# Kernel optimization log

Hardware: AMD Instinct MI355X
Metric: run time of the kernel (lower is better)

The kernel has to match this reference:

```python
import jax, jax.numpy as jnp
import numpy as np

N_HEADS = 16


def setup_inputs() -> dict:
    key = jax.random.key(0)
    k1, k2, k3 = jax.random.split(key, 3)
    B, T, C = 4, 2048, 1024
    x = jax.random.normal(k1, (B, T, C), dtype=jnp.float32)
    # torch nn.Linear weights are (out_features, in_features); y = x @ W.T
    w_in = jax.random.normal(k2, (3 * C, C), dtype=jnp.float32) * 0.02
    w_out = jax.random.normal(k3, (C, C), dtype=jnp.float32) * 0.02
    return {"x": x, "w_in": w_in, "w_out": w_out}


def reference(x, w_in, w_out):
    B, T, C = x.shape
    H = N_HEADS
    hd = C // H

    qkv = x @ w_in.T                      # [B, T, 3C]
    q, k, v = jnp.split(qkv, 3, axis=2)   # each [B, T, C]

    def heads(t):
        return t.reshape(B, T, H, hd).transpose(0, 2, 1, 3)  # [B, H, T, hd]

    q, k, v = heads(q), heads(k), heads(v)

    scale = 1.0 / jnp.sqrt(jnp.float32(hd))
    scores = jnp.einsum('bhqd,bhkd->bhqk', q, k) * scale      # [B, H, T, T]
    causal = jnp.tril(jnp.ones((T, T), dtype=bool))
    scores = jnp.where(causal, scores, -jnp.inf)
    attn = jax.nn.softmax(scores, axis=-1)
    y = jnp.einsum('bhqk,bhkd->bhqd', attn, v)                # [B, H, T, hd]
    y = y.transpose(0, 2, 1, 3).reshape(B, T, C)
    return y @ w_out.T
```

## Files before the change

kernel.cpp:

```cpp
#include <hip/hip_runtime.h>
#include <stdint.h>

#define BB 4
#define TT 2048
#define CC 1024
#define HH 16
#define HD 64
#define C3 3072
#define MM (BB*TT)

typedef __bf16 bf16_t;
typedef bf16_t bf16x8 __attribute__((ext_vector_type(8)));
typedef float f32x4 __attribute__((ext_vector_type(4)));
typedef unsigned short u16;
typedef u16 u16x8 __attribute__((ext_vector_type(8)));
typedef uint32_t u32;

static __device__ __forceinline__ u16 f2bf(float f){
  u32 u = __builtin_bit_cast(u32, f);
  u32 r = (u + 0x7fffu + ((u >> 16) & 1u)) >> 16;
  return (u16)r;
}

static __device__ __forceinline__ f32x4 mfma16(bf16x8 a, bf16x8 b, f32x4 c){
  return __builtin_amdgcn_mfma_f32_16x16x32_bf16(a, b, c, 0, 0, 0);
}

typedef __attribute__((address_space(1))) void* gas_t;
typedef __attribute__((address_space(3))) void* las_t;
static __device__ __forceinline__ void gload16(const void* g, void* l){
  __builtin_amdgcn_global_load_lds((gas_t)g, (las_t)l, 16, 0, 0);
}

__global__ __launch_bounds__(256) void cvt_all(const float* __restrict__ x,
                                               const float* __restrict__ wi,
                                               const float* __restrict__ wo,
                                               u16* __restrict__ out){
  const int n1 = MM*CC/8, n2 = C3*CC/8, n3 = CC*CC/8;
  const int total = n1 + n2 + n3;
  int stride = gridDim.x * blockDim.x;
  for (int i = blockIdx.x * blockDim.x + threadIdx.x; i < total; i += stride){
    const float* src; int k;
    if (i < n1){ src = x; k = i; }
    else if (i < n1 + n2){ src = wi; k = i - n1; }
    else { src = wo; k = i - n1 - n2; }
    const float4* p = (const float4*)src + (size_t)k * 2;
    float4 a = p[0], b = p[1];
    u16x8 o;
    o[0]=f2bf(a.x); o[1]=f2bf(a.y); o[2]=f2bf(a.z); o[3]=f2bf(a.w);
    o[4]=f2bf(b.x); o[5]=f2bf(b.y); o[6]=f2bf(b.z); o[7]=f2bf(b.w);
    *((u16x8*)out + i) = o;
  }
}

template<int OUTBF>
__global__ __launch_bounds__(256) void gemm_bt(const u16* __restrict__ A,
                                               const u16* __restrict__ Bm,
                                               void* __restrict__ Cp,
                                               int M, int N, int K,
                                               int nbx, int cpx){
  __shared__ u16 As[128*64];
  __shared__ u16 Bs[128*64];
  const int bid = blockIdx.x;
  const int nb = (bid & 7) * cpx + (bid >> 3);
  const int by = nb / nbx, bx = nb - by * nbx;
  const int tid  = threadIdx.x;
  const int lane = tid & 63;
  const int w    = tid >> 6;
  const int m0   = by * 128;
  const int n0   = bx * 128;
  const int wm   = (w >> 1) * 64;
  const int wn   = (w & 1) * 64;
  const int lr   = lane & 15;
  const int lg4  = lane >> 4;

  f32x4 acc[4][4] = {};

  const int rq  = tid >> 3;
  const int c8s = ((tid & 7) ^ (rq & 7)) * 8;
  const u16* gA = A  + (size_t)(m0 + rq) * K + c8s;
  const u16* gB = Bm + (size_t)(n0 + rq) * K + c8s;
  char* lA = (char*)As + tid*16;
  char* lB = (char*)Bs + tid*16;

  for (int k0 = 0; k0 < K; k0 += 64){
    #pragma unroll
    for (int q = 0; q < 4; q++){
      gload16(gA + (size_t)(q*32)*K + k0, lA + q*4096);
      gload16(gB + (size_t)(q*32)*K + k0, lB + q*4096);
    }
    __syncthreads();
    #pragma unroll
    for (int kk = 0; kk < 2; kk++){
      bf16x8 af[4], bfr[4];
      #pragma unroll
      for (int m = 0; m < 4; m++){
        int row = wm + m*16 + lr;
        int slot = ((kk<<2) | lg4) ^ (row & 7);
        af[m] = *(const bf16x8*)((const char*)As + row*128 + slot*16);
      }
      #pragma unroll
      for (int n = 0; n < 4; n++){
        int row = wn + n*16 + lr;
        int slot = ((kk<<2) | lg4) ^ (row & 7);
        bfr[n] = *(const bf16x8*)((const char*)Bs + row*128 + slot*16);
      }
      #pragma unroll
      for (int m = 0; m < 4; m++)
        #pragma unroll
        for (int n = 0; n < 4; n++)
          acc[m][n] = mfma16(af[m], bfr[n], acc[m][n]);
    }
    __syncthreads();
  }

  const int cr = lg4 * 4;
  #pragma unroll
  for (int m = 0; m < 4; m++)
    #pragma unroll
    for (int n = 0; n < 4; n++)
      #pragma unroll
      for (int j = 0; j < 4; j++){
        size_t row = (size_t)(m0 + wm + m*16 + cr + j);
        size_t col = (size_t)(n0 + wn + n*16 + lr);
        if (OUTBF) ((u16*)Cp)[row*(size_t)N + col] = f2bf(acc[m][n][j]);
        else       ((float*)Cp)[row*(size_t)N + col] = acc[m][n][j];
      }
}

__global__ __launch_bounds__(256, 2) void attn_fwd(const u16* __restrict__ qkv,
                                                   u16* __restrict__ y){
  __shared__ u16 Kl[2][64*72];
  __shared__ u16 Vt[2][64*72];
  const int bid = blockIdx.x;
  const int tq = bid >> 6;
  const int h = bid & 15, b = (bid >> 4) & 3;
  const int tid = threadIdx.x, lane = tid & 63, w = tid >> 6;
  const int lr = lane & 15, lg = lane >> 4;
  const size_t base = (size_t)b * TT * C3;
  const int qA = tq*64 + w*16;
  const int qB = (31-tq)*64 + w*16;
  const float SC = 0.18033688011112042f;

  bf16x8 qf[2][2];
  {
    const u16* qp0 = qkv + base + (size_t)(qA + lr) * C3 + h*HD;
    qf[0][0] = *(const bf16x8*)(qp0 + lg*8);
    qf[0][1] = *(const bf16x8*)(qp0 + 32 + lg*8);
    const u16* qp1 = qkv + base + (size_t)(qB + lr) * C3 + h*HD;
    qf[1][0] = *(const bf16x8*)(qp1 + lg*8);
    qf[1][1] = *(const bf16x8*)(qp1 + 32 + lg*8);
    #pragma unroll
    for (int m = 0; m < 2; m++)
      #pragma unroll
      for (int i = 0; i < 2; i++)
        #pragma unroll
        for (int e = 0; e < 8; e++)
          qf[m][i][e] = (bf16_t)((float)qf[m][i][e] * SC);
  }

  const int rK = tid >> 3, cK = tid & 7;
  const int rp = tid & 15;
  const int dc = (tid >> 4) & 7;
  const int hf = tid >> 7;
  const u16* gK = qkv + base + (size_t)rK * C3 + CC + h*HD + cK*8;
  const u16* gV = qkv + base + (size_t)(2*rp + 32*hf) * C3 + 2*CC + h*HD + dc*8;

  const int kkey = ((rK >> 3) & 1) << 5;
  const int kw0 = rK*72 + ((cK*8) ^ kkey);
  const int kw1 = (rK+32)*72 + ((cK*8) ^ kkey);
  const int vcol = (2*rp + 32*hf) ^ (8*dc);

  const int rdx = ((lr >> 2) & 1) << 5;
  const int rbase = 8*(lr >> 2) + (lr & 3);

  u16x8 kreg[2], vreg[2];
  kreg[0] = *(const u16x8*)(gK);
  kreg[1] = *(const u16x8*)(gK + (size_t)32*C3);
  vreg[0] = *(const u16x8*)(gV);
  vreg[1] = *(const u16x8*)(gV + C3);

  f32x4 o[2][4] = {};
  float mj[2] = {-1e30f, -1e30f};
  float lj[2] = {0.f, 0.f};

  const int ktmax = 31 - tq;
  for (int kt = 0; kt <= ktmax; kt++){
    const int cb = kt & 1;
    u16* KL = Kl[cb];
    u16* VT = Vt[cb];
    *(u16x8*)&KL[kw0] = kreg[0];
    *(u16x8*)&KL[kw1] = kreg[1];
    #pragma unroll
    for (int e = 0; e < 8; e++){
      u32 pk = (u32)vreg[0][e] | ((u32)vreg[1][e] << 16);
      *(u32*)&VT[(dc*8+e)*72 + vcol] = pk;
    }
    __syncthreads();

    if (kt < ktmax){
      const u16* gk2 = gK + (size_t)(kt+1)*64*C3;
      const u16* gv2 = gV + (size_t)(kt+1)*64*C3;
      kreg[0] = *(const u16x8*)(gk2);
      kreg[1] = *(const u16x8*)(gk2 + (size_t)32*C3);
      vreg[0] = *(const u16x8*)(gv2);
      vreg[1] = *(const u16x8*)(gv2 + C3);
    }

    const bool m0act = (kt <= tq);
    bf16x8 vb[8];

    #pragma unroll
    for (int m = 1; m >= 0; m--){
      if (m == 0 && !m0act) continue;

      f32x4 s[4] = {};
      __builtin_amdgcn_s_setprio(1);
      #pragma unroll
      for (int n = 0; n < 4; n++){
        const int rho = 32*(n>>1) + 4*(n&1) + rbase;
        bf16x8 kb0 = *(const bf16x8*)&KL[rho*72 + ((     lg*8) ^ rdx)];
        bf16x8 kb1 = *(const bf16x8*)&KL[rho*72 + ((32 + lg*8) ^ rdx)];
        s[n] = mfma16(kb0, qf[m][0], s[n]);
        s[n] = mfma16(kb1, qf[m][1], s[n]);
      }
      __builtin_amdgcn_s_setprio(0);

      if (m == 1){
        #pragma unroll
        for (int n = 0; n < 4; n++){
          const int dcr = (2*n + (lr >> 3)) & 7;
          const int c0 = (lg ^ dcr) * 8;
          vb[2*n]   = *(const bf16x8*)&VT[(n*16+lr)*72 + c0];
          vb[2*n+1] = *(const bf16x8*)&VT[(n*16+lr)*72 + (c0 ^ 32)];
        }
      }

      const int qrow = (m ? qB : qA) + lr;
      const bool dm = (kt == (m ? ktmax : tq));
      if (dm){
        #pragma unroll
        for (int n = 0; n < 4; n++)
          #pragma unroll
          for (int j = 0; j < 4; j++)
            if (kt*64 + 32*(n>>1) + 8*lg + 4*(n&1) + j > qrow)
              s[n][j] = -1e30f;
      }
      float x0 = fmaxf(fmaxf(s[0][0], s[0][1]), fmaxf(s[0][2], s[0][3]));
      float x1 = fmaxf(fmaxf(s[1][0], s[1][1]), fmaxf(s[1][2], s[1][3]));
      float x2 = fmaxf(fmaxf(s[2][0], s[2][1]), fmaxf(s[2][2], s[2][3]));
      float x3 = fmaxf(fmaxf(s[3][0], s[3][1]), fmaxf(s[3][2], s[3][3]));
      float tm = fmaxf(fmaxf(x0, x1), fmaxf(x2, x3));
      tm = fmaxf(tm, __shfl_xor(tm, 16, 64));
      tm = fmaxf(tm, __shfl_xor(tm, 32, 64));
      float mo = mj[m];
      if (!__all(tm <= mo + 4.0f)){
        float mn = fmaxf(mo, tm);
        float al = __builtin_amdgcn_exp2f(mo - mn);
        mj[m] = mn;
        lj[m] *= al;
        float a0 = __shfl(al, lg*4+0, 16);
        float a1 = __shfl(al, lg*4+1, 16);
        float a2 = __shfl(al, lg*4+2, 16);
        float a3 = __shfl(al, lg*4+3, 16);
        #pragma unroll
        for (int n = 0; n < 4; n++){
          o[m][n][0] *= a0; o[m][n][1] *= a1;
          o[m][n][2] *= a2; o[m][n][3] *= a3;
        }
      }
      float mm = mj[m];
      float psn[4];
      bf16x8 pa, pb;
      #pragma unroll
      for (int n = 0; n < 4; n++){
        float p0 = __builtin_amdgcn_exp2f(s[n][0] - mm);
        float p1 = __builtin_amdgcn_exp2f(s[n][1] - mm);
        float p2 = __builtin_amdgcn_exp2f(s[n][2] - mm);
        float p3 = __builtin_amdgcn_exp2f(s[n][3] - mm);
        psn[n] = (p0 + p1) + (p2 + p3);
        if (n == 0){ pa[0]=(bf16_t)p0; pa[1]=(bf16_t)p1; pa[2]=(bf16_t)p2; pa[3]=(bf16_t)p3; }
        if (n == 1){ pa[4]=(bf16_t)p0; pa[5]=(bf16_t)p1; pa[6]=(bf16_t)p2; pa[7]=(bf16_t)p3; }
        if (n == 2){ pb[0]=(bf16_t)p0; pb[1]=(bf16_t)p1; pb[2]=(bf16_t)p2; pb[3]=(bf16_t)p3; }
        if (n == 3){ pb[4]=(bf16_t)p0; pb[5]=(bf16_t)p1; pb[6]=(bf16_t)p2; pb[7]=(bf16_t)p3; }
      }
      float ps = (psn[0] + psn[1]) + (psn[2] + psn[3]);
      ps += __shfl_xor(ps, 16, 64);
      ps += __shfl_xor(ps, 32, 64);
      lj[m] += ps;

      __builtin_amdgcn_s_setprio(1);
      #pragma unroll
      for (int n = 0; n < 4; n++){
        o[m][n] = mfma16(pa, vb[2*n],   o[m][n]);
        o[m][n] = mfma16(pb, vb[2*n+1], o[m][n]);
      }
      __builtin_amdgcn_s_setprio(0);
    }
  }

  #pragma unroll
  for (int m = 0; m < 2; m++){
    float inv = 1.0f / lj[m];
    float i0 = __shfl(inv, lg*4+0, 16);
    float i1 = __shfl(inv, lg*4+1, 16);
    float i2 = __shfl(inv, lg*4+2, 16);
    float i3 = __shfl(inv, lg*4+3, 16);
    const int qb = (m ? qB : qA);
    #pragma unroll
    for (int j = 0; j < 4; j++){
      float ij = (j==0) ? i0 : (j==1) ? i1 : (j==2) ? i2 : i3;
      size_t row = (size_t)b*TT + qb + lg*4 + j;
      #pragma unroll
      for (int n = 0; n < 4; n++)
        y[row*CC + h*HD + n*16 + lr] = f2bf(o[m][n][j] * ij);
    }
  }
}

extern "C" void kernel_launch(void* const* d_in, const int* in_sizes, int n_in,
                              void* d_out, int out_size, void* d_ws, size_t ws_size,
                              hipStream_t stream){
  const float* x     = (const float*)d_in[0];
  const float* w_in  = (const float*)d_in[1];
  const float* w_out = (const float*)d_in[2];
  float* out = (float*)d_out;

  u16* xb   = (u16*)d_ws;
  u16* wib  = xb  + (size_t)MM * CC;
  u16* wob  = wib + (size_t)C3 * CC;
  u16* qkvb = wob + (size_t)CC * CC;
  u16* yb   = xb;

  cvt_all<<<2048, 256, 0, stream>>>(x, w_in, w_out, xb);

  gemm_bt<1><<<1536, 256, 0, stream>>>(xb, wib, (void*)qkvb, MM, C3, CC, 24, 192);
  attn_fwd<<<1024, 256, 0, stream>>>(qkvb, yb);
  gemm_bt<0><<<512, 256, 0, stream>>>(yb, wob, (void*)out, MM, CC, CC, 8, 64);
}
```

Before: 165.1 us.

## Use 256x256 double-buffered tile GEMM with 512 threads for QKV projection

Adds a new GEMM kernel for the QKV projection that uses 256x256 output tiles, 8 waves per block, and double-buffered shared memory. Global loads for the next K-tile are interleaved with MFMA phases, and the kernel uses barriers and priority hints. The larger tiles raise arithmetic intensity and cut redundant global reads relative to the 128x128 kernel. The costs are a larger LDS footprint (128KB per block), heavy register use for the 8x4 accumulators, and only 384 blocks, which may underfill 256 CUs at 2 blocks per CU.

Measured after the change: 175.7 us. +6.4%, slower.

```diff
diff --git a/kernel.cpp b/kernel.cpp
--- a/kernel.cpp
+++ b/kernel.cpp
@@ -51,6 +51,110 @@
     o[4]=f2bf(b.x); o[5]=f2bf(b.y); o[6]=f2bf(b.z); o[7]=f2bf(b.w);
     *((u16x8*)out + i) = o;
   }
+}
+
+__global__ __launch_bounds__(512, 2) void gemm_bt256(const u16* __restrict__ A,
+                                                     const u16* __restrict__ Bm,
+                                                     u16* __restrict__ Cp,
+                                                     int N, int K,
+                                                     int nbx, int cpx){
+  __shared__ u16 As[2][256*64];
+  __shared__ u16 Bs[2][256*64];
+  const int bid = blockIdx.x;
+  const int nb = (bid & 7) * cpx + (bid >> 3);
+  const int by = nb / nbx, bx = nb - by * nbx;
+  const int tid = threadIdx.x;
+  const int lane = tid & 63;
+  const int w = tid >> 6;
+  const int m0g = by * 256, n0g = bx * 256;
+  const int wm = (w >> 2) * 128;
+  const int wn = (w & 3) * 64;
+  const int lr = lane & 15;
+  const int lg4 = lane >> 4;
+
+  f32x4 acc[8][4] = {};
+
+  const int rq  = tid >> 3;
+  const int c8s = ((tid & 7) ^ (rq & 7)) * 8;
+  const u16* gA = A  + (size_t)(m0g + rq) * K + c8s;
+  const u16* gB = Bm + (size_t)(n0g + rq) * K + c8s;
+
+  auto stage2 = [&](int buf, int t1, int q){
+    gload16(gA + (size_t)(q*64)*K + t1*64, (char*)&As[buf][0] + q*8192 + tid*16);
+    gload16(gB + (size_t)(q*64)*K + t1*64, (char*)&Bs[buf][0] + q*8192 + tid*16);
+  };
+  auto lda = [&](int buf, int m, int kk)->bf16x8{
+    int row = wm + m*16 + lr;
+    int slot = ((kk<<2) | lg4) ^ (row & 7);
+    return *(const bf16x8*)((const char*)&As[buf][0] + row*128 + slot*16);
+  };
+  auto ldb = [&](int buf, int n, int kk)->bf16x8{
+    int row = wn + n*16 + lr;
+    int slot = ((kk<<2) | lg4) ^ (row & 7);
+    return *(const bf16x8*)((const char*)&Bs[buf][0] + row*128 + slot*16);
+  };
+
+  #pragma unroll
+  for (int q = 0; q < 4; q++) stage2(0, 0, q);
+
+  const int NT = K >> 6;
+  for (int t = 0; t < NT; t++){
+    const int c = t & 1;
+    const bool pf = (t + 1 < NT);
+    bf16x8 bfr[4][2];
+
+    if (pf){ stage2(c^1, t+1, 0); asm volatile("s_waitcnt vmcnt(2)" ::: "memory"); }
+    else   {                      asm volatile("s_waitcnt vmcnt(0)" ::: "memory"); }
+    __builtin_amdgcn_s_barrier();
+    __builtin_amdgcn_sched_barrier(0);
+    #pragma unroll
+    for (int n = 0; n < 4; n++){ bfr[n][0] = ldb(c,n,0); bfr[n][1] = ldb(c,n,1); }
+    {
+      bf16x8 a00 = lda(c,0,0), a01 = lda(c,0,1);
+      bf16x8 a10 = lda(c,1,0), a11 = lda(c,1,1);
+      __builtin_amdgcn_s_setprio(1);
+      #pragma unroll
+      for (int n = 0; n < 4; n++){
+        acc[0][n] = mfma16(a00, bfr[n][0], acc[0][n]);
+        acc[0][n] = mfma16(a01, bfr[n][1], acc[0][n]);
+        acc[1][n] = mfma16(a10, bfr[n][0], acc[1][n]);
+        acc[1][n] = mfma16(a11, bfr[n][1], acc[1][n]);
+      }
+      __builtin_amdgcn_s_setprio(0);
+    }
+    __builtin_amdgcn_s_barrier();
+
+    #pragma unroll
+    for (int p = 1; p < 4; p++){
+      bf16x8 a00 = lda(c,2*p,0),   a01 = lda(c,2*p,1);
+      bf16x8 a10 = lda(c,2*p+1,0), a11 = lda(c,2*p+1,1);
+      if (pf) stage2(c^1, t+1, p);
+      __builtin_amdgcn_s_barrier();
+      __builtin_amdgcn_sched_barrier(0);
+      __builtin_amdgcn_s_setprio(1);
+      #pragma unroll
+      for (int n = 0; n < 4; n++){
+        acc[2*p][n]   = mfma16(a00, bfr[n][0], acc[2*p][n]);
+        acc[2*p][n]   = mfma16(a01, bfr[n][1], acc[2*p][n]);
+        acc[2*p+1][n] = mfma16(a10, bfr[n][0], acc[2*p+1][n]);
+        acc[2*p+1][n] = mfma16(a11, bfr[n][1], acc[2*p+1][n]);
+      }
+      __builtin_amdgcn_s_setprio(0);
+      __builtin_amdgcn_s_barrier();
+    }
+  }
+
+  const int cr = lg4 * 4;
+  #pragma unroll
+  for (int m = 0; m < 8; m++)
+    #pragma unroll
+    for (int n = 0; n < 4; n++)
+      #pragma unroll
+      for (int j = 0; j < 4; j++){
+        size_t row = (size_t)(m0g + wm + m*16 + cr + j);
+        size_t col = (size_t)(n0g + wn + n*16 + lr);
+        Cp[row*(size_t)N + col] = f2bf(acc[m][n][j]);
+      }
 }
 
 template<int OUTBF>
@@ -334,7 +438,7 @@
 
   cvt_all<<<2048, 256, 0, stream>>>(x, w_in, w_out, xb);
 
-  gemm_bt<1><<<1536, 256, 0, stream>>>(xb, wib, (void*)qkvb, MM, C3, CC, 24, 192);
+  gemm_bt256<<<384, 512, 0, stream>>>(xb, wib, qkvb, C3, CC, 12, 48);
   attn_fwd<<<1024, 256, 0, stream>>>(qkvb, yb);
   gemm_bt<0><<<512, 256, 0, stream>>>(yb, wob, (void*)out, MM, CC, CC, 8, 64);
 }
```

## Stage two K/V tiles per barrier in attention loop

Applied to the files above, without the earlier changes.

The attention kernel now moves two 64-key tiles of K and V into shared memory per loop iteration, double-buffered, instead of one. The goal is to halve the number of block-wide barriers and to issue larger, deeper global prefetches that overlap more with compute. In exchange, shared memory per block doubles to about 74 KB and prefetch register use doubles. That may lower occupancy or cause register spills under the two-blocks-per-CU launch bound. When the number of key tiles is odd, the last iteration also loads one extra tile it never uses.

Result: slower. 168.4 us (+2.0%).

```diff
diff --git a/kernel.cpp b/kernel.cpp
--- a/kernel.cpp
+++ b/kernel.cpp
@@ -130,8 +130,8 @@
 
 __global__ __launch_bounds__(256, 2) void attn_fwd(const u16* __restrict__ qkv,
                                                    u16* __restrict__ y){
-  __shared__ u16 Kl[2][64*72];
-  __shared__ u16 Vt[2][64*72];
+  __shared__ u16 Kl[2][2][64*72];
+  __shared__ u16 Vt[2][2][64*72];
   const int bid = blockIdx.x;
   const int tq = bid >> 6;
   const int h = bid & 15, b = (bid >> 4) & 3;
@@ -174,128 +174,145 @@
   const int rdx = ((lr >> 2) & 1) << 5;
   const int rbase = 8*(lr >> 2) + (lr & 3);
 
-  u16x8 kreg[2], vreg[2];
-  kreg[0] = *(const u16x8*)(gK);
-  kreg[1] = *(const u16x8*)(gK + (size_t)32*C3);
-  vreg[0] = *(const u16x8*)(gV);
-  vreg[1] = *(const u16x8*)(gV + C3);
+  u16x8 kreg[2][2], vreg[2][2];
+  #pragma unroll
+  for (int st = 0; st < 2; st++){
+    const size_t o64 = (size_t)(st*64) * C3;
+    kreg[st][0] = *(const u16x8*)(gK + o64);
+    kreg[st][1] = *(const u16x8*)(gK + o64 + (size_t)32*C3);
+    vreg[st][0] = *(const u16x8*)(gV + o64);
+    vreg[st][1] = *(const u16x8*)(gV + o64 + C3);
+  }
 
   f32x4 o[2][4] = {};
   float mj[2] = {-1e30f, -1e30f};
   float lj[2] = {0.f, 0.f};
 
   const int ktmax = 31 - tq;
-  for (int kt = 0; kt <= ktmax; kt++){
-    const int cb = kt & 1;
-    u16* KL = Kl[cb];
-    u16* VT = Vt[cb];
-    *(u16x8*)&KL[kw0] = kreg[0];
-    *(u16x8*)&KL[kw1] = kreg[1];
-    #pragma unroll
-    for (int e = 0; e < 8; e++){
-      u32 pk = (u32)vreg[0][e] | ((u32)vreg[1][e] << 16);
-      *(u32*)&VT[(dc*8+e)*72 + vcol] = pk;
+  const int NIT = (ktmax >> 1) + 1;
+  for (int it = 0; it < NIT; it++){
+    const int cb = it & 1;
+    #pragma unroll
+    for (int st = 0; st < 2; st++){
+      u16* KL = &Kl[cb][st][0];
+      u16* VT = &Vt[cb][st][0];
+      *(u16x8*)&KL[kw0] = kreg[st][0];
+      *(u16x8*)&KL[kw1] = kreg[st][1];
+      #pragma unroll
+      for (int e = 0; e < 8; e++){
+        u32 pk = (u32)vreg[st][0][e] | ((u32)vreg[st][1][e] << 16);
+        *(u32*)&VT[(dc*8+e)*72 + vcol] = pk;
+      }
     }
     __syncthreads();
 
-    if (kt < ktmax){
-      const u16* gk2 = gK + (size_t)(kt+1)*64*C3;
-      const u16* gv2 = gV + (size_t)(kt+1)*64*C3;
-      kreg[0] = *(const u16x8*)(gk2);
-      kreg[1] = *(const u16x8*)(gk2 + (size_t)32*C3);
-      vreg[0] = *(const u16x8*)(gv2);
-      vreg[1] = *(const u16x8*)(gv2 + C3);
-    }
-
-    const bool m0act = (kt <= tq);
-    bf16x8 vb[8];
-
-    #pragma unroll
-    for (int m = 1; m >= 0; m--){
-      if (m == 0 && !m0act) continue;
-
-      f32x4 s[4] = {};
-      __builtin_amdgcn_s_setprio(1);
-      #pragma unroll
-      for (int n = 0; n < 4; n++){
-        const int rho = 32*(n>>1) + 4*(n&1) + rbase;
-        bf16x8 kb0 = *(const bf16x8*)&KL[rho*72 + ((     lg*8) ^ rdx)];
-        bf16x8 kb1 = *(const bf16x8*)&KL[rho*72 + ((32 + lg*8) ^ rdx)];
-        s[n] = mfma16(kb0, qf[m][0], s[n]);
-        s[n] = mfma16(kb1, qf[m][1], s[n]);
-      }
-      __builtin_amdgcn_s_setprio(0);
-
-      if (m == 1){
+    if (it + 1 < NIT){
+      #pragma unroll
+      for (int st = 0; st < 2; st++){
+        const size_t o2 = (size_t)((it+1)*128 + st*64) * C3;
+        kreg[st][0] = *(const u16x8*)(gK + o2);
+        kreg[st][1] = *(const u16x8*)(gK + o2 + (size_t)32*C3);
+        vreg[st][0] = *(const u16x8*)(gV + o2);
+        vreg[st][1] = *(const u16x8*)(gV + o2 + C3);
+      }
+    }
+
+    #pragma unroll
+    for (int st = 0; st < 2; st++){
+      const int kst = 2*it + st;
+      if (kst > ktmax) continue;
+      const u16* KL = &Kl[cb][st][0];
+      const u16* VT = &Vt[cb][st][0];
+      const bool m0act = (kst <= tq);
+      bf16x8 vb[8];
+
+      #pragma unroll
+      for (int m = 1; m >= 0; m--){
+        if (m == 0 && !m0act) continue;
+
+        f32x4 s[4] = {};
+        __builtin_amdgcn_s_setprio(1);
         #pragma unroll
         for (int n = 0; n < 4; n++){
-          const int dcr = (2*n + (lr >> 3)) & 7;
-          const int c0 = (lg ^ dcr) * 8;
-          vb[2*n]   = *(const bf16x8*)&VT[(n*16+lr)*72 + c0];
-          vb[2*n+1] = *(const bf16x8*)&VT[(n*16+lr)*72 + (c0 ^ 32)];
-        }
-      }
-
-      const int qrow = (m ? qB : qA) + lr;
-      const bool dm = (kt == (m ? ktmax : tq));
-      if (dm){
-        #pragma unroll
-        for (int n = 0; n < 4; n++)
+          const int rho = 32*(n>>1) + 4*(n&1) + rbase;
+          bf16x8 kb0 = *(const bf16x8*)&KL[rho*72 + ((     lg*8) ^ rdx)];
+          bf16x8 kb1 = *(const bf16x8*)&KL[rho*72 + ((32 + lg*8) ^ rdx)];
+          s[n] = mfma16(kb0, qf[m][0], s[n]);
+          s[n] = mfma16(kb1, qf[m][1], s[n]);
+        }
+        __builtin_amdgcn_s_setprio(0);
+
+        if (m == 1){
           #pragma unroll
-          for (int j = 0; j < 4; j++)
-            if (kt*64 + 32*(n>>1) + 8*lg + 4*(n&1) + j > qrow)
-              s[n][j] = -1e30f;
-      }
-      float x0 = fmaxf(fmaxf(s[0][0], s[0][1]), fmaxf(s[0][2], s[0][3]));
-      float x1 = fmaxf(fmaxf(s[1][0], s[1][1]), fmaxf(s[1][2], s[1][3]));
-      float x2 = fmaxf(fmaxf(s[2][0], s[2][1]), fmaxf(s[2][2], s[2][3]));
-      float x3 = fmaxf(fmaxf(s[3][0], s[3][1]), fmaxf(s[3][2], s[3][3]));
-      float tm = fmaxf(fmaxf(x0, x1), fmaxf(x2, x3));
-      tm = fmaxf(tm, __shfl_xor(tm, 16, 64));
-      tm = fmaxf(tm, __shfl_xor(tm, 32, 64));
-      float mo = mj[m];
-      if (!__all(tm <= mo + 4.0f)){
-        float mn = fmaxf(mo, tm);
-        float al = __builtin_amdgcn_exp2f(mo - mn);
-        mj[m] = mn;
-        lj[m] *= al;
-        float a0 = __shfl(al, lg*4+0, 16);
-        float a1 = __shfl(al, lg*4+1, 16);
-        float a2 = __shfl(al, lg*4+2, 16);
-        float a3 = __shfl(al, lg*4+3, 16);
+          for (int n = 0; n < 4; n++){
+            const int dcr = (2*n + (lr >> 3)) & 7;
+            const int c0 = (lg ^ dcr) * 8;
+            vb[2*n]   = *(const bf16x8*)&VT[(n*16+lr)*72 + c0];
+            vb[2*n+1] = *(const bf16x8*)&VT[(n*16+lr)*72 + (c0 ^ 32)];
+          }
+        }
+
+        const int qrow = (m ? qB : qA) + lr;
+        const bool dm = (kst == (m ? ktmax : tq));
+        if (dm){
+          #pragma unroll
+          for (int n = 0; n < 4; n++)
+            #pragma unroll
+            for (int j = 0; j < 4; j++)
+              if (kst*64 + 32*(n>>1) + 8*lg + 4*(n&1) + j > qrow)
+                s[n][j] = -1e30f;
+        }
+        float x0 = fmaxf(fmaxf(s[0][0], s[0][1]), fmaxf(s[0][2], s[0][3]));
+        float x1 = fmaxf(fmaxf(s[1][0], s[1][1]), fmaxf(s[1][2], s[1][3]));
+        float x2 = fmaxf(fmaxf(s[2][0], s[2][1]), fmaxf(s[2][2], s[2][3]));
+        float x3 = fmaxf(fmaxf(s[3][0], s[3][1]), fmaxf(s[3][2], s[3][3]));
+        float tm = fmaxf(fmaxf(x0, x1), fmaxf(x2, x3));
+        tm = fmaxf(tm, __shfl_xor(tm, 16, 64));
+        tm = fmaxf(tm, __shfl_xor(tm, 32, 64));
+        float mo = mj[m];
+        if (!__all(tm <= mo + 4.0f)){
+          float mn = fmaxf(mo, tm);
+          float al = __builtin_amdgcn_exp2f(mo - mn);
+          mj[m] = mn;
+          lj[m] *= al;
+          float a0 = __shfl(al, lg*4+0, 16);
+          float a1 = __shfl(al, lg*4+1, 16);
+          float a2 = __shfl(al, lg*4+2, 16);
+          float a3 = __shfl(al, lg*4+3, 16);
+          #pragma unroll
+          for (int n = 0; n < 4; n++){
+            o[m][n][0] *= a0; o[m][n][1] *= a1;
+            o[m][n][2] *= a2; o[m][n][3] *= a3;
+          }
+        }
+        float mm = mj[m];
+        float psn[4];
+        bf16x8 pa, pb;
         #pragma unroll
         for (int n = 0; n < 4; n++){
-          o[m][n][0] *= a0; o[m][n][1] *= a1;
-          o[m][n][2] *= a2; o[m][n][3] *= a3;
-        }
-      }
-      float mm = mj[m];
-      float psn[4];
-      bf16x8 pa, pb;
-      #pragma unroll
-      for (int n = 0; n < 4; n++){
-        float p0 = __builtin_amdgcn_exp2f(s[n][0] - mm);
-        float p1 = __builtin_amdgcn_exp2f(s[n][1] - mm);
-        float p2 = __builtin_amdgcn_exp2f(s[n][2] - mm);
-        float p3 = __builtin_amdgcn_exp2f(s[n][3] - mm);
-        psn[n] = (p0 + p1) + (p2 + p3);
-        if (n == 0){ pa[0]=(bf16_t)p0; pa[1]=(bf16_t)p1; pa[2]=(bf16_t)p2; pa[3]=(bf16_t)p3; }
-        if (n == 1){ pa[4]=(bf16_t)p0; pa[5]=(bf16_t)p1; pa[6]=(bf16_t)p2; pa[7]=(bf16_t)p3; }
-        if (n == 2){ pb[0]=(bf16_t)p0; pb[1]=(bf16_t)p1; pb[2]=(bf16_t)p2; pb[3]=(bf16_t)p3; }
-        if (n == 3){ pb[4]=(bf16_t)p0; pb[5]=(bf16_t)p1; pb[6]=(bf16_t)p2; pb[7]=(bf16_t)p3; }
-      }
-      float ps = (psn[0] + psn[1]) + (psn[2] + psn[3]);
-      ps += __shfl_xor(ps, 16, 64);
-      ps += __shfl_xor(ps, 32, 64);
-      lj[m] += ps;
-
-      __builtin_amdgcn_s_setprio(1);
-      #pragma unroll
-      for (int n = 0; n < 4; n++){
-        o[m][n] = mfma16(pa, vb[2*n],   o[m][n]);
-        o[m][n] = mfma16(pb, vb[2*n+1], o[m][n]);
-      }
-      __builtin_amdgcn_s_setprio(0);
+          float p0 = __builtin_amdgcn_exp2f(s[n][0] - mm);
+          float p1 = __builtin_amdgcn_exp2f(s[n][1] - mm);
+          float p2 = __builtin_amdgcn_exp2f(s[n][2] - mm);
+          float p3 = __builtin_amdgcn_exp2f(s[n][3] - mm);
+          psn[n] = (p0 + p1) + (p2 + p3);
+          if (n == 0){ pa[0]=(bf16_t)p0; pa[1]=(bf16_t)p1; pa[2]=(bf16_t)p2; pa[3]=(bf16_t)p3; }
+          if (n == 1){ pa[4]=(bf16_t)p0; pa[5]=(bf16_t)p1; pa[6]=(bf16_t)p2; pa[7]=(bf16_t)p3; }
+          if (n == 2){ pb[0]=(bf16_t)p0; pb[1]=(bf16_t)p1; pb[2]=(bf16_t)p2; pb[3]=(bf16_t)p3; }
+          if (n == 3){ pb[4]=(bf16_t)p0; pb[5]=(bf16_t)p1; pb[6]=(bf16_t)p2; pb[7]=(bf16_t)p3; }
+        }
+        float ps = (psn[0] + psn[1]) + (psn[2] + psn[3]);
+        ps += __shfl_xor(ps, 16, 64);
+        ps += __shfl_xor(ps, 32, 64);
+        lj[m] += ps;
+
+        __builtin_amdgcn_s_setprio(1);
+        #pragma unroll
+        for (int n = 0; n < 4; n++){
+          o[m][n] = mfma16(pa, vb[2*n],   o[m][n]);
+          o[m][n] = mfma16(pb, vb[2*n+1], o[m][n]);
+        }
+        __builtin_amdgcn_s_setprio(0);
+      }
     }
   }
 
```
